# Kernel tuning notes

Hardware: AMD Instinct MI355X
Metric: run time of the kernel (lower is better)

Reference implementation:

```python
import jax, jax.numpy as jnp
import numpy as np

FILTER_SIZE = 5
C_IN = 32
C_OUT = 64
N = 8192


def setup_inputs() -> dict:
    key = jax.random.key(0)
    k1, k2, k3 = jax.random.split(key, 3)
    L = jax.random.normal(k1, (N, N), dtype=jnp.float32) / np.float32(np.sqrt(N))
    x = jax.random.normal(k2, (C_IN, N), dtype=jnp.float32)
    theta = jax.random.normal(k3, (C_OUT, C_IN, FILTER_SIZE), dtype=jnp.float32)  # variance=1.0
    bias = jnp.zeros((C_OUT, 1), dtype=jnp.float32)
    return {"L": L, "x": x, "theta": theta, "bias": bias}


def reference(L, x, theta, bias):
    # Chebyshev recurrence vectorized over all input channels at once.
    # Original does per-channel column matvecs L @ x[c]; here T_k has shape
    # (C_in, N) and L @ x_col per channel == T @ L.T.
    T_prev = x                      # T_0, (C_in, N)
    Ts = [T_prev]
    if FILTER_SIZE > 1:
        T_curr = T_prev @ L.T       # T_1
        Ts.append(T_curr)
        for _ in range(2, FILTER_SIZE):
            T_next = 2.0 * (T_curr @ L.T) - T_prev
            Ts.append(T_next)
            T_prev, T_curr = T_curr, T_next
    X = jnp.stack(Ts, axis=-1)      # (C_in, N, K) — matches torch assemble
    y = jnp.einsum('imk,oik->om', X, theta) + bias  # (C_out, N)
    return y
```

## Files before the change

### kernel.cpp

```cpp
#include <hip/hip_runtime.h>

#define NN 8192
#define CIN 32
#define COUT 64
#define KF 5

typedef __attribute__((ext_vector_type(8))) short bf16x8_t;
typedef __attribute__((ext_vector_type(4))) float f32x4_t;

typedef const __attribute__((address_space(1))) void* as1_t;
typedef __attribute__((address_space(3))) void* as3_t;
__device__ __forceinline__ void gll16(const void* g, void* l) {
    __builtin_amdgcn_global_load_lds((as1_t)g, (as3_t)l, 16, 0, 0);
}

__device__ __forceinline__ short f2bf(float f) {
    unsigned u = __builtin_bit_cast(unsigned, f);
    unsigned r = (u + 0x7FFFu + ((u >> 16) & 1u)) >> 16;
    return (short)(unsigned short)r;
}

__device__ __forceinline__ bf16x8_t cvt8v(f32x4_t a, f32x4_t b) {
    bf16x8_t v;
    v[0] = f2bf(a[0]); v[1] = f2bf(a[1]); v[2] = f2bf(a[2]); v[3] = f2bf(a[3]);
    v[4] = f2bf(b[0]); v[5] = f2bf(b[1]); v[6] = f2bf(b[2]); v[7] = f2bf(b[3]);
    return v;
}

__global__ void cvt_kernel(const float* __restrict__ src, short* __restrict__ dst) {
    int idx = blockIdx.x * 256 + threadIdx.x;
    float4 v = reinterpret_cast<const float4*>(src)[idx];
    short4 o;
    o.x = f2bf(v.x); o.y = f2bf(v.y); o.z = f2bf(v.z); o.w = f2bf(v.w);
    reinterpret_cast<short4*>(dst)[idx] = o;
}

__device__ __forceinline__ void stash_partials(float* red, int wave, int g, int r,
                                               const f32x4_t& acc0, const f32x4_t& acc1) {
    const int base = wave * 512 + g * 64 + r;
#pragma unroll
    for (int t = 0; t < 4; ++t) {
        red[base + t * 16]       = acc0[t];
        red[base + t * 16 + 256] = acc1[t];
    }
}

__device__ __forceinline__ float reduce8(const float* red, int tid) {
    float s = red[tid];
#pragma unroll
    for (int w = 1; w < 8; ++w) s += red[w * 512 + tid];
    return s;
}

__global__ __launch_bounds__(512, 8) void pass1_kernel(
    const float* __restrict__ L, const short* __restrict__ Tb0,
    char* __restrict__ LbC, float* __restrict__ part)
{
    __shared__ float red[4096];
    const int tid = threadIdx.x, wave = tid >> 6, lane = tid & 63;
    const int g = lane >> 4, r = lane & 15;
    const int t = blockIdx.x >> 1, h = blockIdx.x & 1;
    const int i0 = t * 16;
    const int kw = h * 4096 + wave * 512;

    const float* Lrow = L   + (size_t)(i0 + r) * NN + kw + g * 8;
    const short* A0   = Tb0 + (size_t)r * NN        + kw + g * 8;
    const short* A1   = Tb0 + (size_t)(r + 16) * NN + kw + g * 8;
    char* LbW = LbC + (size_t)t * 262144 + (size_t)(h * 4 + (wave >> 1)) * 32768
              + (wave & 1) * 16384 + lane * 16;

    f32x4_t acc0 = {0.f,0.f,0.f,0.f}, acc1 = {0.f,0.f,0.f,0.f};
    for (int it = 0; it < 16; ++it) {
        const int jl = it * 32;
        f32x4_t l0 = __builtin_nontemporal_load(reinterpret_cast<const f32x4_t*>(Lrow + jl));
        f32x4_t l1 = __builtin_nontemporal_load(reinterpret_cast<const f32x4_t*>(Lrow + jl) + 1);
        bf16x8_t a0 = *(const bf16x8_t*)(A0 + jl);
        bf16x8_t a1 = *(const bf16x8_t*)(A1 + jl);
        bf16x8_t b = cvt8v(l0, l1);
        *(bf16x8_t*)(LbW + it * 1024) = b;
        acc0 = __builtin_amdgcn_mfma_f32_16x16x32_bf16(a0, b, acc0, 0, 0, 0);
        acc1 = __builtin_amdgcn_mfma_f32_16x16x32_bf16(a1, b, acc1, 0, 0, 0);
    }

    stash_partials(red, wave, g, r, acc0, acc1);
    __syncthreads();
    const int c = tid >> 4, il = tid & 15;
    part[(size_t)h * CIN * NN + (size_t)c * NN + i0 + il] = reduce8(red, tid);
}

__global__ __launch_bounds__(256) void combine1_kernel(
    const float* __restrict__ part, float* __restrict__ Tf1, short* __restrict__ Tb1)
{
    const int idx = blockIdx.x * 256 + threadIdx.x;
    const float4 p0 = reinterpret_cast<const float4*>(part)[idx];
    const float4 p1 = reinterpret_cast<const float4*>(part + (size_t)CIN * NN)[idx];
    float4 v;
    v.x = p0.x + p1.x; v.y = p0.y + p1.y; v.z = p0.z + p1.z; v.w = p0.w + p1.w;
    reinterpret_cast<float4*>(Tf1)[idx] = v;
    short4 b;
    b.x = f2bf(v.x); b.y = f2bf(v.y); b.z = f2bf(v.z); b.w = f2bf(v.w);
    reinterpret_cast<short4*>(Tb1)[idx] = b;
}

__device__ __forceinline__ void mid_core(const char* __restrict__ LbW,
                                         const short* __restrict__ Abase,
                                         int wave, int lane, char* stg,
                                         f32x4_t& acc0, f32x4_t& acc1)
{
    const int g = lane >> 4, r = lane & 15;
    const int kw = wave * 1024;
    const char* srcL = LbW + lane * 16;
    const short* A0 = Abase + (size_t)r * NN        + kw + g * 8;
    const short* A1 = Abase + (size_t)(r + 16) * NN + kw + g * 8;

    gll16(srcL + 0,    stg + 0);
    gll16(srcL + 1024, stg + 1024);
    gll16(srcL + 2048, stg + 2048);
    gll16(srcL + 3072, stg + 3072);

    for (int c = 0; c < 16; ++c) {
        if (c < 15) asm volatile("s_waitcnt vmcnt(2)" ::: "memory");
        else        asm volatile("s_waitcnt vmcnt(0)" ::: "memory");
        const char* Ld = stg + (c & 1) * 2048;
#pragma unroll
        for (int kk = 0; kk < 2; ++kk) {
            bf16x8_t b  = *(const bf16x8_t*)(Ld + (kk * 4 + g) * 256 + r * 16);
            bf16x8_t a0 = *(const bf16x8_t*)(A0 + c * 64 + kk * 32);
            bf16x8_t a1 = *(const bf16x8_t*)(A1 + c * 64 + kk * 32);
            acc0 = __builtin_amdgcn_mfma_f32_16x16x32_bf16(a0, b, acc0, 0, 0, 0);
            acc1 = __builtin_amdgcn_mfma_f32_16x16x32_bf16(a1, b, acc1, 0, 0, 0);
        }
        if (c < 14) {
            asm volatile("s_waitcnt lgkmcnt(0)" ::: "memory");
            const int cn = c + 2;
            gll16(srcL + cn * 2048,        stg + (cn & 1) * 2048);
            gll16(srcL + cn * 2048 + 1024, stg + (cn & 1) * 2048 + 1024);
        }
    }
}

__global__ __launch_bounds__(512, 4) void passmid_kernel(
    const char* __restrict__ LbC, const short* __restrict__ A,
    const float* __restrict__ Tprev, float* __restrict__ Tf, short* __restrict__ Tb)
{
    __shared__ float red[4096];
    __shared__ __align__(16) char stg[8][4096];
    const int tid = threadIdx.x, wave = tid >> 6, lane = tid & 63;
    const int g = lane >> 4, r = lane & 15;
    const int t = blockIdx.x, i0 = t * 16;

    f32x4_t acc0 = {0.f,0.f,0.f,0.f}, acc1 = {0.f,0.f,0.f,0.f};
    mid_core(LbC + (size_t)t * 262144 + wave * 32768, A, wave, lane, stg[wave], acc0, acc1);

    stash_partials(red, wave, g, r, acc0, acc1);
    __syncthreads();
    const int c = tid >> 4, il = tid & 15;
    const size_t off = (size_t)c * NN + i0 + il;
    const float val = 2.0f * reduce8(red, tid) - Tprev[off];
    Tf[off] = val;
    Tb[off] = f2bf(val);
}

__global__ __launch_bounds__(512, 4) void pass4_kernel(
    const char* __restrict__ LbC, const short* __restrict__ A,
    const float* __restrict__ Tf2, const float* __restrict__ x,
    const float* __restrict__ Tf1, const float* __restrict__ Tf3,
    const float* __restrict__ theta, const float* __restrict__ bias,
    float* __restrict__ y)
{
    __shared__ float red[4096];
    __shared__ __align__(16) char stg[8][4096];
    const int tid = threadIdx.x, wave = tid >> 6, lane = tid & 63;
    const int g = lane >> 4, r = lane & 15;
    const int t = blockIdx.x, i0 = t * 16;

    f32x4_t acc0 = {0.f,0.f,0.f,0.f}, acc1 = {0.f,0.f,0.f,0.f};
    mid_core(LbC + (size_t)t * 262144 + wave * 32768, A, wave, lane, stg[wave], acc0, acc1);

    stash_partials(red, wave, g, r, acc0, acc1);
    __syncthreads();
    {
        const int c = tid >> 4, il = tid & 15;
        red[tid] = 2.0f * reduce8(red, tid) - Tf2[(size_t)c * NN + i0 + il];
    }
    __syncthreads();

    const int o = tid >> 4, il = tid & 15;
    float a0 = bias[o], a1 = bias[o + 32];
    for (int cc = 0; cc < CIN; ++cc) {
        const size_t off = (size_t)cc * NN + i0 + il;
        const float t0 = x[off], t1 = Tf1[off], t2 = Tf2[off], t3 = Tf3[off];
        const float t4 = red[cc * 16 + il];
        const float* th0 = theta + ((size_t)o * CIN + cc) * KF;
        const float* th1 = theta + ((size_t)(o + 32) * CIN + cc) * KF;
        a0 += t0 * th0[0] + t1 * th0[1] + t2 * th0[2] + t3 * th0[3] + t4 * th0[4];
        a1 += t0 * th1[0] + t1 * th1[1] + t2 * th1[2] + t3 * th1[3] + t4 * th1[4];
    }
    y[(size_t)o * NN + i0 + il]        = a0;
    y[(size_t)(o + 32) * NN + i0 + il] = a1;
}

extern "C" void kernel_launch(void* const* d_in, const int* in_sizes, int n_in,
                              void* d_out, int out_size, void* d_ws, size_t ws_size,
                              hipStream_t stream) {
    const float* L     = (const float*)d_in[0];
    const float* x     = (const float*)d_in[1];
    const float* theta = (const float*)d_in[2];
    const float* bias  = (const float*)d_in[3];
    float* y = (float*)d_out;

    const size_t TE = (size_t)CIN * NN;
    const size_t LE = (size_t)NN * NN;

    char*  LbC = (char*)d_ws;
    float* Tf1 = (float*)(LbC + LE * 2);
    float* Tf2 = Tf1 + TE;
    float* Tf3 = Tf2 + TE;
    short* Tb0 = (short*)(Tf3 + TE);
    short* Tb1 = Tb0 + TE;
    short* Tb2 = Tb1 + TE;
    short* Tb3 = Tb2 + TE;
    float* part = (float*)(Tb3 + TE);

    cvt_kernel<<<256, 256, 0, stream>>>(x, Tb0);
    pass1_kernel<<<NN / 8, 512, 0, stream>>>(L, Tb0, LbC, part);
    combine1_kernel<<<256, 256, 0, stream>>>(part, Tf1, Tb1);
    passmid_kernel<<<NN / 16, 512, 0, stream>>>(LbC, Tb1, x,   Tf2, Tb2);
    passmid_kernel<<<NN / 16, 512, 0, stream>>>(LbC, Tb2, Tf1, Tf3, Tb3);
    pass4_kernel<<<NN / 16, 512, 0, stream>>>(LbC, Tb3, Tf2, x, Tf1, Tf3,
                                              theta, bias, y);
}
```

Before: 244.6 us.

## Stage L conversion through swizzled LDS for coalesced loads and bf16 image writes

Pass 1 now reads each row of L with fully coalesced 16-byte loads, converts to bf16 into a swizzled 32KB LDS image, and writes that image to the bf16 copy of L with contiguous 16-byte stores. The MFMAs then read their operands from LDS. Previously each lane read strided row segments and scattered 16-byte stores. The K dimension is split 8 ways instead of 2, giving 4096 blocks and needing an 8-way partial-sum combine. The cost is more partial traffic and extra LDS use per block, which lowers occupancy.

Result: faster. 218.9 us, median of 2 (-10.5%).

```diff
diff --git a/kernel.cpp b/kernel.cpp
--- a/kernel.cpp
+++ b/kernel.cpp
@@ -18,13 +18,6 @@
     unsigned u = __builtin_bit_cast(unsigned, f);
     unsigned r = (u + 0x7FFFu + ((u >> 16) & 1u)) >> 16;
     return (short)(unsigned short)r;
-}
-
-__device__ __forceinline__ bf16x8_t cvt8v(f32x4_t a, f32x4_t b) {
-    bf16x8_t v;
-    v[0] = f2bf(a[0]); v[1] = f2bf(a[1]); v[2] = f2bf(a[2]); v[3] = f2bf(a[3]);
-    v[4] = f2bf(b[0]); v[5] = f2bf(b[1]); v[6] = f2bf(b[2]); v[7] = f2bf(b[3]);
-    return v;
 }
 
 __global__ void cvt_kernel(const float* __restrict__ src, short* __restrict__ dst) {
@@ -52,53 +45,90 @@
     return s;
 }
 
-__global__ __launch_bounds__(512, 8) void pass1_kernel(
+__global__ __launch_bounds__(512, 2) void pass1_kernel(
     const float* __restrict__ L, const short* __restrict__ Tb0,
     char* __restrict__ LbC, float* __restrict__ part)
 {
     __shared__ float red[4096];
+    __shared__ __align__(16) char img[32768];
     const int tid = threadIdx.x, wave = tid >> 6, lane = tid & 63;
-    const int g = lane >> 4, r = lane & 15;
-    const int t = blockIdx.x >> 1, h = blockIdx.x & 1;
-    const int i0 = t * 16;
-    const int kw = h * 4096 + wave * 512;
-
-    const float* Lrow = L   + (size_t)(i0 + r) * NN + kw + g * 8;
-    const short* A0   = Tb0 + (size_t)r * NN        + kw + g * 8;
-    const short* A1   = Tb0 + (size_t)(r + 16) * NN + kw + g * 8;
-    char* LbW = LbC + (size_t)t * 262144 + (size_t)(h * 4 + (wave >> 1)) * 32768
-              + (wave & 1) * 16384 + lane * 16;
-
+    const int t = blockIdx.x >> 3, p = blockIdx.x & 7;
+    const int i0 = t * 16, kp = p * 1024;
+
+    {
+        const int chunk_lo = lane >> 4;
+        const int kk = (lane >> 3) & 1;
+        const int g = (lane >> 1) & 3;
+        const int half = (lane & 1) * 8;
+#pragma unroll
+        for (int rr = 0; rr < 2; ++rr) {
+            const int r = wave * 2 + rr;
+            const float* src = L + (size_t)(i0 + r) * NN + kp + lane * 4;
+#pragma unroll
+            for (int seg = 0; seg < 4; ++seg) {
+                f32x4_t v = __builtin_nontemporal_load(
+                    reinterpret_cast<const f32x4_t*>(src + seg * 256));
+                short4 b4;
+                b4.x = f2bf(v[0]); b4.y = f2bf(v[1]); b4.z = f2bf(v[2]); b4.w = f2bf(v[3]);
+                const int chunk = seg * 4 + chunk_lo;
+                const int byte = chunk * 2048 + kk * 1024 + g * 256 + r * 16 + half;
+                const int sw = byte ^ (((byte >> 8) & 0xF) << 4);
+                *reinterpret_cast<short4*>(img + sw) = b4;
+            }
+        }
+    }
+    __syncthreads();
+
+    {
+        char* dst = LbC + (size_t)t * 262144 + p * 32768;
+#pragma unroll
+        for (int i = 0; i < 4; ++i) {
+            const int b = tid * 16 + i * 8192;
+            const int sw = b ^ (((b >> 8) & 0xF) << 4);
+            *reinterpret_cast<f32x4_t*>(dst + b) =
+                *reinterpret_cast<const f32x4_t*>(img + sw);
+        }
+    }
+
+    const int g = lane >> 4, r = lane & 15;
+    const short* A0 = Tb0 + (size_t)r * NN + kp;
+    const short* A1 = Tb0 + (size_t)(r + 16) * NN + kp;
     f32x4_t acc0 = {0.f,0.f,0.f,0.f}, acc1 = {0.f,0.f,0.f,0.f};
-    for (int it = 0; it < 16; ++it) {
-        const int jl = it * 32;
-        f32x4_t l0 = __builtin_nontemporal_load(reinterpret_cast<const f32x4_t*>(Lrow + jl));
-        f32x4_t l1 = __builtin_nontemporal_load(reinterpret_cast<const f32x4_t*>(Lrow + jl) + 1);
-        bf16x8_t a0 = *(const bf16x8_t*)(A0 + jl);
-        bf16x8_t a1 = *(const bf16x8_t*)(A1 + jl);
-        bf16x8_t b = cvt8v(l0, l1);
-        *(bf16x8_t*)(LbW + it * 1024) = b;
-        acc0 = __builtin_amdgcn_mfma_f32_16x16x32_bf16(a0, b, acc0, 0, 0, 0);
-        acc1 = __builtin_amdgcn_mfma_f32_16x16x32_bf16(a1, b, acc1, 0, 0, 0);
-    }
-
+#pragma unroll
+    for (int cc = 0; cc < 2; ++cc) {
+        const int chunk = wave * 2 + cc;
+#pragma unroll
+        for (int kk = 0; kk < 2; ++kk) {
+            const int byte = chunk * 2048 + kk * 1024 + g * 256 + r * 16;
+            const int sw = byte ^ (((byte >> 8) & 0xF) << 4);
+            bf16x8_t b = *reinterpret_cast<const bf16x8_t*>(img + sw);
+            const int ja = chunk * 64 + kk * 32 + g * 8;
+            bf16x8_t a0 = *reinterpret_cast<const bf16x8_t*>(A0 + ja);
+            bf16x8_t a1 = *reinterpret_cast<const bf16x8_t*>(A1 + ja);
+            acc0 = __builtin_amdgcn_mfma_f32_16x16x32_bf16(a0, b, acc0, 0, 0, 0);
+            acc1 = __builtin_amdgcn_mfma_f32_16x16x32_bf16(a1, b, acc1, 0, 0, 0);
+        }
+    }
     stash_partials(red, wave, g, r, acc0, acc1);
     __syncthreads();
     const int c = tid >> 4, il = tid & 15;
-    part[(size_t)h * CIN * NN + (size_t)c * NN + i0 + il] = reduce8(red, tid);
-}
-
-__global__ __launch_bounds__(256) void combine1_kernel(
+    part[(size_t)p * CIN * NN + (size_t)c * NN + i0 + il] = reduce8(red, tid);
+}
+
+__global__ __launch_bounds__(256) void combine8_kernel(
     const float* __restrict__ part, float* __restrict__ Tf1, short* __restrict__ Tb1)
 {
     const int idx = blockIdx.x * 256 + threadIdx.x;
-    const float4 p0 = reinterpret_cast<const float4*>(part)[idx];
-    const float4 p1 = reinterpret_cast<const float4*>(part + (size_t)CIN * NN)[idx];
-    float4 v;
-    v.x = p0.x + p1.x; v.y = p0.y + p1.y; v.z = p0.z + p1.z; v.w = p0.w + p1.w;
-    reinterpret_cast<float4*>(Tf1)[idx] = v;
+    const int NQ = CIN * NN / 4;
+    float4 s = reinterpret_cast<const float4*>(part)[idx];
+#pragma unroll
+    for (int t = 1; t < 8; ++t) {
+        float4 v = reinterpret_cast<const float4*>(part)[(size_t)t * NQ + idx];
+        s.x += v.x; s.y += v.y; s.z += v.z; s.w += v.w;
+    }
+    reinterpret_cast<float4*>(Tf1)[idx] = s;
     short4 b;
-    b.x = f2bf(v.x); b.y = f2bf(v.y); b.z = f2bf(v.z); b.w = f2bf(v.w);
+    b.x = f2bf(s.x); b.y = f2bf(s.y); b.z = f2bf(s.z); b.w = f2bf(s.w);
     reinterpret_cast<short4*>(Tb1)[idx] = b;
 }
 
@@ -223,8 +253,8 @@
     float* part = (float*)(Tb3 + TE);
 
     cvt_kernel<<<256, 256, 0, stream>>>(x, Tb0);
-    pass1_kernel<<<NN / 8, 512, 0, stream>>>(L, Tb0, LbC, part);
-    combine1_kernel<<<256, 256, 0, stream>>>(part, Tf1, Tb1);
+    pass1_kernel<<<(NN / 16) * 8, 512, 0, stream>>>(L, Tb0, LbC, part);
+    combine8_kernel<<<256, 256, 0, stream>>>(part, Tf1, Tb1);
     passmid_kernel<<<NN / 16, 512, 0, stream>>>(LbC, Tb1, x,   Tf2, Tb2);
     passmid_kernel<<<NN / 16, 512, 0, stream>>>(LbC, Tb2, Tf1, Tf3, Tb3);
     pass4_kernel<<<NN / 16, 512, 0, stream>>>(LbC, Tb3, Tf2, x, Tf1, Tf3,
```
